# Kernel tuning notes

Hardware: AMD Instinct MI355X
Metric: run time of the kernel (lower is better)

The kernel has to match this reference:

```python
import jax, jax.numpy as jnp
import numpy as np

N = 100000
E = 1600000
H = 128
M = 256
L = 6
G = 512          # number of graphs in the batch
A = 95           # num_atom_types
EXTRA = 3        # input_dim - 1
EPS = 1e-5


def swish(x):
    return x * jax.nn.sigmoid(x)


def setup_inputs() -> dict:
    key = jax.random.key(0)
    ks = jax.random.split(key, 16)
    z = jax.random.randint(ks[0], (N, 1), 0, A).astype(jnp.float32)
    extra = jax.random.normal(ks[1], (N, EXTRA), dtype=jnp.float32)
    x = jnp.concatenate([z, extra], axis=1)                     # [N, 4]
    edge_index = jax.random.randint(ks[2], (2, E), 0, N)        # [2, E]
    batch = jnp.sort(jax.random.randint(ks[3], (N,), 0, G))     # [N]
    s = 0.02
    z_embed = jax.random.normal(ks[4], (A, H), dtype=jnp.float32) * s
    extra_w = jax.random.normal(ks[5], (H, EXTRA), dtype=jnp.float32) * (1.0 / np.sqrt(EXTRA))
    extra_b = jnp.zeros((H,), jnp.float32)
    conv_w = jax.random.normal(ks[6], (L, H, H), dtype=jnp.float32) * (1.0 / np.sqrt(H))
    conv_b = jnp.zeros((L, H), jnp.float32)
    gamma = jnp.ones((L, H), jnp.float32)
    beta = jnp.zeros((L, H), jnp.float32)
    mean_scale = jnp.ones((L, H), jnp.float32)
    mlp_w1 = jax.random.normal(ks[7], (L, M, H), dtype=jnp.float32) * (1.0 / np.sqrt(H))
    mlp_b1 = jnp.zeros((L, M), jnp.float32)
    mlp_w2 = jax.random.normal(ks[8], (L, H, M), dtype=jnp.float32) * (1.0 / np.sqrt(M))
    mlp_b2 = jnp.zeros((L, H), jnp.float32)
    return dict(x=x, edge_index=edge_index, batch=batch, z_embed=z_embed,
                extra_w=extra_w, extra_b=extra_b, conv_w=conv_w, conv_b=conv_b,
                gamma=gamma, beta=beta, mean_scale=mean_scale,
                mlp_w1=mlp_w1, mlp_b1=mlp_b1, mlp_w2=mlp_w2, mlp_b2=mlp_b2)


def gnn_forward(x, edge_index, batch, z_embed, extra_w, extra_b, conv_w, conv_b,
                gamma, beta, mean_scale, mlp_w1, mlp_b1, mlp_w2, mlp_b2):
    z = x[:, 0].astype(jnp.int32)
    h = z_embed[z] + x[:, 1:] @ extra_w.T + extra_b                 # [N, H]

    # GCN: add self loops, symmetric normalization (computed once; graph is static)
    loop = jnp.arange(N)
    src = jnp.concatenate([edge_index[0], loop])
    dst = jnp.concatenate([edge_index[1], loop])
    deg = jax.ops.segment_sum(jnp.ones_like(dst, jnp.float32), dst, num_segments=N)
    dinv = jnp.where(deg > 0, jax.lax.rsqrt(jnp.maximum(deg, 1.0)), 0.0)
    norm = (dinv[src] * dinv[dst])[:, None]                         # [E+N, 1]

    cnt = jax.ops.segment_sum(jnp.ones((N,), jnp.float32), batch, num_segments=G)[:, None]
    cnt = jnp.maximum(cnt, 1.0)

    for i in range(L):
        h_res = h
        # GCNConv
        xw = h @ conv_w[i].T
        agg = jax.ops.segment_sum(xw[src] * norm, dst, num_segments=N) + conv_b[i]
        # GraphNorm: gamma * (x - alpha*mean) / sqrt(var + eps) + beta, per graph
        mean = jax.ops.segment_sum(agg, batch, num_segments=G) / cnt   # [G, H]
        sub = agg - mean_scale[i] * mean[batch]
        var = jax.ops.segment_sum(sub * sub, batch, num_segments=G) / cnt
        hn = gamma[i] * sub * jax.lax.rsqrt(var[batch] + EPS) + beta[i]
        ha = swish(hn)
        # residual MLP
        h = swish(swish(ha @ mlp_w1[i].T + mlp_b1[i]) @ mlp_w2[i].T + mlp_b2[i]) + h_res
    return h


def reference(x, edge_index, batch, z_embed, extra_w, extra_b, conv_w, conv_b,
              gamma, beta, mean_scale, mlp_w1, mlp_b1, mlp_w2, mlp_b2):
    return gnn_forward(x, edge_index, batch, z_embed, extra_w, extra_b, conv_w, conv_b,
                       gamma, beta, mean_scale, mlp_w1, mlp_b1, mlp_w2, mlp_b2)
```

## Files before the change

kernel.cpp:

```cpp
#include <hip/hip_runtime.h>

#define NN 100000
#define EE 1600000
#define HH 128
#define MM 256
#define LL 6
#define GG 512
#define SCAN_NB ((NN + 1023) / 1024)

typedef __attribute__((ext_vector_type(8))) short short8;
typedef __attribute__((ext_vector_type(4))) float floatx4;

__device__ __forceinline__ float swishf(float v) {
    return v * __builtin_amdgcn_rcpf(1.0f + __expf(-v));
}

__device__ __forceinline__ unsigned short f2bf(float f) {
    unsigned u = __builtin_bit_cast(unsigned, f);
    unsigned r = u + 0x7FFFu + ((u >> 16) & 1u);
    return (unsigned short)(r >> 16);
}

__device__ __forceinline__ float bf2f(unsigned short u) {
    return __builtin_bit_cast(float, (unsigned)u << 16);
}

__device__ __forceinline__ float2 bf2f2(unsigned u) {
    float2 r;
    r.x = __builtin_bit_cast(float, u << 16);
    r.y = __builtin_bit_cast(float, u & 0xFFFF0000u);
    return r;
}

__device__ __forceinline__ unsigned cvt2bf(float a, float b) {
    unsigned r;
    asm("v_cvt_pk_bf16_f32 %0, %1, %2" : "=v"(r) : "v"(a), "v"(b));
    return r;
}

__device__ __forceinline__ void unpack8(uint4 v, float* a) {
    float2 p0 = bf2f2(v.x), p1 = bf2f2(v.y), p2 = bf2f2(v.z), p3 = bf2f2(v.w);
    a[0] = p0.x; a[1] = p0.y; a[2] = p1.x; a[3] = p1.y;
    a[4] = p2.x; a[5] = p2.y; a[6] = p3.x; a[7] = p3.y;
}

__device__ __forceinline__ uint4 pack8(const float* o) {
    uint4 pk;
    pk.x = cvt2bf(o[0], o[1]);
    pk.y = cvt2bf(o[2], o[3]);
    pk.z = cvt2bf(o[4], o[5]);
    pk.w = cvt2bf(o[6], o[7]);
    return pk;
}

__device__ __forceinline__ uint2 pack4(const float* o) {
    uint2 pk;
    pk.x = cvt2bf(o[0], o[1]);
    pk.y = cvt2bf(o[2], o[3]);
    return pk;
}

__global__ void k_embed(const float* __restrict__ x, const float* __restrict__ z_embed,
                        const float* __restrict__ ew, const float* __restrict__ eb,
                        unsigned short* __restrict__ hb) {
    int idx = blockIdx.x * blockDim.x + threadIdx.x;
    if (idx >= NN * 32) return;
    int n = idx >> 5;
    int c0 = (idx & 31) << 2;
    const float* xr = x + (size_t)n * 4;
    int z = (int)xr[0];
    float x1 = xr[1], x2 = xr[2], x3 = xr[3];
    const float* ze = z_embed + (size_t)z * HH + c0;
    float o[4];
#pragma unroll
    for (int j = 0; j < 4; ++j) {
        int c = c0 + j;
        o[j] = ze[j] + x1 * ew[c * 3 + 0] + x2 * ew[c * 3 + 1] + x3 * ew[c * 3 + 2] + eb[c];
    }
    *(uint2*)(hb + (size_t)n * HH + c0) = pack4(o);
}

__global__ void k_f2bf3(const float* __restrict__ s1, unsigned short* __restrict__ d1, int n1,
                        const float* __restrict__ s2, unsigned short* __restrict__ d2, int n2,
                        const float* __restrict__ s3, unsigned short* __restrict__ d3, int n3) {
    int i = blockIdx.x * blockDim.x + threadIdx.x;
    if (i < n1) {
        d1[i] = f2bf(s1[i]);
    } else if (i < n1 + n2) {
        d2[i - n1] = f2bf(s2[i - n1]);
    } else if (i < n1 + n2 + n3) {
        d3[i - n1 - n2] = f2bf(s3[i - n1 - n2]);
    }
}

__global__ __launch_bounds__(256) void k_degree_p(const int* __restrict__ dst,
                                                  int* __restrict__ deg) {
    int part = blockIdx.x & 7;
    int blk = blockIdx.x >> 3;
    int nb = gridDim.x >> 3;
    int lo = (int)((long long)part * NN / 8);
    int hi = (int)((long long)(part + 1) * NN / 8);
    for (int e = blk * 256 + threadIdx.x; e < EE; e += nb * 256) {
        int d = dst[e];
        if (d >= lo && d < hi) atomicAdd(&deg[d], 1);
    }
}

__global__ void k_scan1(const int* __restrict__ deg, int* __restrict__ bsum,
                        float* __restrict__ dinv) {
    __shared__ int sd[256];
    int t = threadIdx.x;
    int base = blockIdx.x * 1024 + t * 4;
    int s = 0;
#pragma unroll
    for (int j = 0; j < 4; ++j) {
        int i = base + j;
        if (i < NN) {
            int dg = deg[i];
            s += dg;
            dinv[i] = rsqrtf((float)(dg + 1));
        }
    }
    sd[t] = s;
    __syncthreads();
    for (int off = 128; off > 0; off >>= 1) {
        if (t < off) sd[t] += sd[t + off];
        __syncthreads();
    }
    if (t == 0) bsum[blockIdx.x] = sd[0];
}

__global__ void k_scan2(const int* __restrict__ bsum, int* __restrict__ boff) {
    __shared__ int sd[128];
    int t = threadIdx.x;
    int v = (t < SCAN_NB) ? bsum[t] : 0;
    sd[t] = v;
    __syncthreads();
    for (int off = 1; off < 128; off <<= 1) {
        int u = (t >= off) ? sd[t - off] : 0;
        __syncthreads();
        sd[t] += u;
        __syncthreads();
    }
    boff[t] = sd[t] - v;
}

__global__ void k_scan3(const int* __restrict__ deg, const int* __restrict__ boff,
                        int* __restrict__ rowptr) {
    __shared__ int sd[256];
    int t = threadIdx.x;
    int base = blockIdx.x * 1024 + t * 4;
    int v[4];
    int s = 0;
#pragma unroll
    for (int j = 0; j < 4; ++j) {
        int i = base + j;
        v[j] = (i < NN) ? deg[i] : 0;
        s += v[j];
    }
    sd[t] = s;
    __syncthreads();
    for (int off = 1; off < 256; off <<= 1) {
        int u = (t >= off) ? sd[t - off] : 0;
        __syncthreads();
        sd[t] += u;
        __syncthreads();
    }
    int run = boff[blockIdx.x] + sd[t] - s;
#pragma unroll
    for (int j = 0; j < 4; ++j) {
        int i = base + j;
        if (i < NN) rowptr[i] = run;
        if (i == NN - 1) rowptr[NN] = run + v[j];
        run += v[j];
    }
}

__global__ __launch_bounds__(256) void k_fill_p(const int* __restrict__ ei,
                                                const int* __restrict__ rowptr,
                                                int* __restrict__ cursor,
                                                int* __restrict__ col) {
    int part = blockIdx.x & 7;
    int blk = blockIdx.x >> 3;
    int nb = gridDim.x >> 3;
    int lo = (int)((long long)part * NN / 8);
    int hi = (int)((long long)(part + 1) * NN / 8);
    for (int e = blk * 256 + threadIdx.x; e < EE; e += nb * 256) {
        int d = ei[EE + e];
        if (d >= lo && d < hi) {
            int p = atomicAdd(&cursor[d], 1);
            col[rowptr[d] + p] = ei[e];
        }
    }
}

__global__ void k_gptr(const int* __restrict__ batch, int* __restrict__ gptr) {
    int n = blockIdx.x * blockDim.x + threadIdx.x;
    if (n >= NN) return;
    int b = batch[n];
    int pb = (n == 0) ? -1 : batch[n - 1];
    for (int g = pb + 1; g <= b; ++g) gptr[g] = n;
    if (n == NN - 1) {
        for (int g = b + 1; g <= GG; ++g) gptr[g] = NN;
    }
}

__global__ __launch_bounds__(256) void k_conv(const unsigned short* __restrict__ A,
                                              const unsigned short* __restrict__ B,
                                              const float* __restrict__ dinv,
                                              unsigned short* __restrict__ Cb) {
    __shared__ unsigned short Bs[128][HH + 8];
    const int tid = threadIdx.x;
    const int wave = tid >> 6;
    const int lane = tid & 63;
    const int quad = lane >> 4;
    const int l16 = lane & 15;
    const int wr = (wave & 1) << 6;
    const int wc = (wave >> 1) << 6;
    const int rowBase = blockIdx.x * 128;

    for (int i = tid; i < 128 * (HH / 8); i += 256) {
        int r = i / (HH / 8);
        int kk = (i % (HH / 8)) * 8;
        int rho = (r & 64) | ((r & 3) << 4) | ((r >> 2) & 15);
        *(uint4*)(&Bs[rho][kk]) = *(const uint4*)(B + (size_t)r * HH + kk);
    }

    floatx4 acc[4][4];
    const floatx4 zed = {0.f, 0.f, 0.f, 0.f};
#pragma unroll
    for (int i = 0; i < 4; ++i)
#pragma unroll
        for (int j = 0; j < 4; ++j) acc[i][j] = zed;

    int ar[4];
#pragma unroll
    for (int i = 0; i < 4; ++i) {
        int r = rowBase + wr + (i << 4) + l16;
        ar[i] = r < NN ? r : NN - 1;
    }

    __syncthreads();

#pragma unroll
    for (int ks = 0; ks < HH / 32; ++ks) {
        int k = (ks << 5) + (quad << 3);
        short8 a[4], b[4];
#pragma unroll
        for (int i = 0; i < 4; ++i) a[i] = *(const short8*)(A + (size_t)ar[i] * HH + k);
#pragma unroll
        for (int j = 0; j < 4; ++j) b[j] = *(const short8*)(&Bs[wc + (j << 4) + l16][k]);
#pragma unroll
        for (int i = 0; i < 4; ++i)
#pragma unroll
            for (int j = 0; j < 4; ++j)
                acc[i][j] =
                    __builtin_amdgcn_mfma_f32_16x16x32_bf16(a[i], b[j], acc[i][j], 0, 0, 0);
    }

    const int c0 = wc + (l16 << 2);
#pragma unroll
    for (int i = 0; i < 4; ++i) {
        int rb = rowBase + wr + (i << 4) + (quad << 2);
#pragma unroll
        for (int reg = 0; reg < 4; ++reg) {
            int r = rb + reg;
            if (r < NN) {
                float dv = dinv[r];
                float o[4];
#pragma unroll
                for (int j = 0; j < 4; ++j) o[j] = acc[i][j][reg] * dv;
                *(uint2*)(Cb + (size_t)r * HH + c0) = pack4(o);
            }
        }
    }
}

__global__ __launch_bounds__(256) void k_agg(const unsigned short* __restrict__ y,
                                             const int* __restrict__ rowptr,
                                             const int* __restrict__ col,
                                             const float* __restrict__ dinv,
                                             const float* __restrict__ cb,
                                             const int* __restrict__ batch,
                                             unsigned short* __restrict__ agg,
                                             float* __restrict__ S1g,
                                             float* __restrict__ S2g) {
    __shared__ float s1s[4][128];
    __shared__ float s2s[4][128];
    __shared__ int sg[4];
    int w = threadIdx.x >> 6;
    int lane = threadIdx.x & 63;
    int grp = lane >> 4;
    int l16 = lane & 15;
    const uint4* yv = (const uint4*)y;
    const int dbase = blockIdx.x * 16 + w * 4;

    float cbv[8];
    {
        float4 c0 = *(const float4*)(cb + l16 * 8);
        float4 c1 = *(const float4*)(cb + l16 * 8 + 4);
        cbv[0] = c0.x; cbv[1] = c0.y; cbv[2] = c0.z; cbv[3] = c0.w;
        cbv[4] = c1.x; cbv[5] = c1.y; cbv[6] = c1.z; cbv[7] = c1.w;
    }

    float sA[8], sB[8];
#pragma unroll
    for (int j = 0; j < 8; ++j) { sA[j] = 0.f; sB[j] = 0.f; }
    int gcur = -1;

    for (int i = 0; i < 4; ++i) {
        int d = dbase + i;
        float acc[8];
#pragma unroll
        for (int j = 0; j < 8; ++j) acc[j] = 0.f;
        if (grp == 0) {
            uint4 v = yv[(size_t)d * 16 + l16];
            unpack8(v, acc);
        }
        int beg = rowptr[d];
        int end = rowptr[d + 1];
        int e = beg + grp;
        for (; e + 4 < end; e += 8) {
            int s0 = col[e];
            int s1 = col[e + 4];
            uint4 v0 = yv[(size_t)s0 * 16 + l16];
            uint4 v1 = yv[(size_t)s1 * 16 + l16];
            float b0[8], b1[8];
            unpack8(v0, b0);
            unpack8(v1, b1);
#pragma unroll
            for (int k = 0; k < 8; ++k) acc[k] += (b0[k] + b1[k]);
        }
        if (e < end) {
            int s0 = col[e];
            uint4 v0 = yv[(size_t)s0 * 16 + l16];
            float b0[8];
            unpack8(v0, b0);
#pragma unroll
            for (int k = 0; k < 8; ++k) acc[k] += b0[k];
        }
#pragma unroll
        for (int j = 0; j < 8; ++j) {
            acc[j] += __shfl_xor(acc[j], 16, 64);
            acc[j] += __shfl_xor(acc[j], 32, 64);
        }
        if (grp == 0) {
            float dv = dinv[d];
            float o[8];
#pragma unroll
            for (int j = 0; j < 8; ++j) o[j] = acc[j] * dv + cbv[j];
            uint4 pk = pack8(o);
            *(uint4*)(agg + (size_t)d * HH + l16 * 8) = pk;
            float2 q0 = bf2f2(pk.x), q1 = bf2f2(pk.y), q2 = bf2f2(pk.z), q3 = bf2f2(pk.w);
            float orv[8] = {q0.x, q0.y, q1.x, q1.y, q2.x, q2.y, q3.x, q3.y};
            int g = batch[d];
            if (g != gcur) {
                if (gcur >= 0) {
#pragma unroll
                    for (int j = 0; j < 8; ++j) {
                        atomicAdd(&S1g[gcur * HH + l16 * 8 + j], sA[j]);
                        atomicAdd(&S2g[gcur * HH + l16 * 8 + j], sB[j]);
                    }
                }
                gcur = g;
#pragma unroll
                for (int j = 0; j < 8; ++j) {
                    sA[j] = orv[j];
                    sB[j] = orv[j] * orv[j];
                }
            } else {
#pragma unroll
                for (int j = 0; j < 8; ++j) {
                    sA[j] += orv[j];
                    sB[j] += orv[j] * orv[j];
                }
            }
        }
    }

    if (grp == 0) {
#pragma unroll
        for (int j = 0; j < 8; ++j) {
            s1s[w][l16 * 8 + j] = sA[j];
            s2s[w][l16 * 8 + j] = sB[j];
        }
        if (l16 == 0) sg[w] = gcur;
    }
    __syncthreads();
    if (threadIdx.x < 128) {
        int c = threadIdx.x;
        int g0 = sg[0], g1 = sg[1], g2 = sg[2], g3 = sg[3];
        if (g0 >= 0 && g0 == g1 && g0 == g2 && g0 == g3) {
            float a = (s1s[0][c] + s1s[1][c]) + (s1s[2][c] + s1s[3][c]);
            float b = (s2s[0][c] + s2s[1][c]) + (s2s[2][c] + s2s[3][c]);
            atomicAdd(&S1g[g0 * HH + c], a);
            atomicAdd(&S2g[g0 * HH + c], b);
        } else {
            int gs[4] = {g0, g1, g2, g3};
#pragma unroll
            for (int ww = 0; ww < 4; ++ww) {
                if (gs[ww] >= 0) {
                    atomicAdd(&S1g[gs[ww] * HH + c], s1s[ww][c]);
                    atomicAdd(&S2g[gs[ww] * HH + c], s2s[ww][c]);
                }
            }
        }
    }
}

__global__ __launch_bounds__(128) void k_finalize(const int* __restrict__ gptr,
                                                  const float* __restrict__ ms,
                                                  const float* __restrict__ gamma,
                                                  const float* __restrict__ beta,
                                                  const float* __restrict__ S1g,
                                                  const float* __restrict__ S2g,
                                                  float* __restrict__ c1,
                                                  float* __restrict__ c0) {
    int g = blockIdx.x;
    int c = threadIdx.x;
    int cnt = gptr[g + 1] - gptr[g];
    float inv = 1.0f / (float)(cnt > 0 ? cnt : 1);
    float S1 = S1g[g * HH + c];
    float S2 = S2g[g * HH + c];
    float m = S1 * inv;
    float msc = ms[c];
    float var = S2 * inv - msc * (2.0f - msc) * m * m;
    float rstd = rsqrtf(var + 1e-5f);
    float c1v = gamma[c] * rstd;
    c1[g * HH + c] = c1v;
    c0[g * HH + c] = beta[c] - c1v * msc * m;
}

__global__ __launch_bounds__(256, 4) void k_mega(const unsigned short* __restrict__ agg,
                                                 const int* __restrict__ batch,
                                                 const float* __restrict__ c1,
                                                 const float* __restrict__ c0,
                                                 const unsigned short* __restrict__ W1,
                                                 const float* __restrict__ b1,
                                                 const unsigned short* __restrict__ W2,
                                                 const float* __restrict__ b2,
                                                 const unsigned short* __restrict__ Wc,
                                                 const float* __restrict__ dinv,
                                                 unsigned short* __restrict__ hb,
                                                 float* __restrict__ h_out,
                                                 unsigned short* __restrict__ y_out,
                                                 int writeF, int doConv) {
    __shared__ unsigned short ha_s[64 * 136];
    __shared__ unsigned short ts[64 * 136];
    const int tid = threadIdx.x;
    const int wave = tid >> 6;
    const int lane = tid & 63;
    const int quad = lane >> 4;
    const int l16 = lane & 15;
    const int rowBase = blockIdx.x * 64;
    const floatx4 zed = {0.f, 0.f, 0.f, 0.f};

    const int wrb = (wave & 1) << 5;
    const int wcb = (wave >> 1) << 6;
    const int co = wcb + (l16 << 2);

    {
        int lr = tid >> 2;
        int coff = (tid & 3) << 5;
        int r = rowBase + lr;
        if (r >= NN) r = NN - 1;
        int g = batch[r];
        const float* c1p = c1 + g * HH + coff;
        const float* c0p = c0 + g * HH + coff;
#pragma unroll
        for (int q = 0; q < 4; ++q) {
            uint4 raw = *(const uint4*)(agg + (size_t)r * HH + coff + (q << 3));
            float v[8];
            unpack8(raw, v);
            float4 ca = *(const float4*)(c1p + (q << 3));
            float4 cb4 = *(const float4*)(c1p + (q << 3) + 4);
            float4 da = *(const float4*)(c0p + (q << 3));
            float4 db = *(const float4*)(c0p + (q << 3) + 4);
            float cc1[8] = {ca.x, ca.y, ca.z, ca.w, cb4.x, cb4.y, cb4.z, cb4.w};
            float cc0[8] = {da.x, da.y, da.z, da.w, db.x, db.y, db.z, db.w};
            float o[8];
#pragma unroll
            for (int j = 0; j < 8; ++j) o[j] = swishf(cc1[j] * v[j] + cc0[j]);
            *(uint4*)(&ha_s[lr * 136 + coff + (q << 3)]) = pack8(o);
        }
    }
    __syncthreads();

    {
        floatx4 acc2[2][4];
#pragma unroll
        for (int i = 0; i < 2; ++i)
#pragma unroll
            for (int j = 0; j < 4; ++j) acc2[i][j] = zed;

#pragma unroll
        for (int h = 0; h < 2; ++h) {
            floatx4 acc1[4][2];
#pragma unroll
            for (int i = 0; i < 4; ++i)
#pragma unroll
                for (int j = 0; j < 2; ++j) acc1[i][j] = zed;
            const int tcol = (wave << 5) + (l16 << 1);
#pragma unroll
            for (int ks = 0; ks < 4; ++ks) {
                int k = (ks << 5) + (quad << 3);
                short8 a[4], b[2];
#pragma unroll
                for (int i = 0; i < 4; ++i)
                    a[i] = *(const short8*)(&ha_s[((i << 4) + l16) * 136 + k]);
#pragma unroll
                for (int j = 0; j < 2; ++j)
                    b[j] = *(const short8*)(W1 + (size_t)((h << 7) + tcol + j) * HH + k);
#pragma unroll
                for (int i = 0; i < 4; ++i)
#pragma unroll
                    for (int j = 0; j < 2; ++j)
                        acc1[i][j] = __builtin_amdgcn_mfma_f32_16x16x32_bf16(a[i], b[j],
                                                                             acc1[i][j], 0, 0, 0);
            }
            float2 bv = *(const float2*)(b1 + (h << 7) + tcol);
#pragma unroll
            for (int i = 0; i < 4; ++i) {
#pragma unroll
                for (int reg = 0; reg < 4; ++reg) {
                    int lr = (i << 4) + (quad << 2) + reg;
                    float o0 = swishf(acc1[i][0][reg] + bv.x);
                    float o1 = swishf(acc1[i][1][reg] + bv.y);
                    *(unsigned*)(&ts[lr * 136 + tcol]) = cvt2bf(o0, o1);
                }
            }
            __syncthreads();

#pragma unroll
            for (int ks = 0; ks < 4; ++ks) {
                int k = (ks << 5) + (quad << 3);
                short8 a[2], b[4];
#pragma unroll
                for (int i = 0; i < 2; ++i)
                    a[i] = *(const short8*)(&ts[(wrb + (i << 4) + l16) * 136 + k]);
#pragma unroll
                for (int j = 0; j < 4; ++j)
                    b[j] = *(const short8*)(W2 + (size_t)(wcb + (l16 << 2) + j) * MM +
                                            (h << 7) + k);
#pragma unroll
                for (int i = 0; i < 2; ++i)
#pragma unroll
                    for (int j = 0; j < 4; ++j)
                        acc2[i][j] = __builtin_amdgcn_mfma_f32_16x16x32_bf16(a[i], b[j],
                                                                             acc2[i][j], 0, 0, 0);
            }
            if (h == 0) __syncthreads();
        }

        float4 b4 = *(const float4*)(b2 + co);
        float bv[4] = {b4.x, b4.y, b4.z, b4.w};
#pragma unroll
        for (int i = 0; i < 2; ++i) {
#pragma unroll
            for (int reg = 0; reg < 4; ++reg) {
                int lr = wrb + (i << 4) + (quad << 2) + reg;
                int r = rowBase + lr;
                if (r < NN) {
                    uint2 rv = *(const uint2*)(hb + (size_t)r * HH + co);
                    float2 r01 = bf2f2(rv.x), r23 = bf2f2(rv.y);
                    float o[4];
                    o[0] = swishf(acc2[i][0][reg] + bv[0]) + r01.x;
                    o[1] = swishf(acc2[i][1][reg] + bv[1]) + r01.y;
                    o[2] = swishf(acc2[i][2][reg] + bv[2]) + r23.x;
                    o[3] = swishf(acc2[i][3][reg] + bv[3]) + r23.y;
                    if (doConv) {
                        uint2 pk = pack4(o);
                        *(uint2*)(hb + (size_t)r * HH + co) = pk;
                        *(uint2*)(&ha_s[lr * 136 + co]) = pk;
                    } else {
                        *(float4*)(h_out + (size_t)r * HH + co) =
                            make_float4(o[0], o[1], o[2], o[3]);
                    }
                } else if (doConv) {
                    *(uint2*)(&ha_s[lr * 136 + co]) = make_uint2(0u, 0u);
                }
            }
        }
    }

    if (doConv) {
        __syncthreads();
        floatx4 acc3[2][4];
#pragma unroll
        for (int i = 0; i < 2; ++i)
#pragma unroll
            for (int j = 0; j < 4; ++j) acc3[i][j] = zed;
#pragma unroll
        for (int ks = 0; ks < 4; ++ks) {
            int k = (ks << 5) + (quad << 3);
            short8 a[2], b[4];
#pragma unroll
            for (int i = 0; i < 2; ++i)
                a[i] = *(const short8*)(&ha_s[(wrb + (i << 4) + l16) * 136 + k]);
#pragma unroll
            for (int j = 0; j < 4; ++j)
                b[j] = *(const short8*)(Wc + (size_t)(wcb + (l16 << 2) + j) * HH + k);
#pragma unroll
            for (int i = 0; i < 2; ++i)
#pragma unroll
                for (int j = 0; j < 4; ++j)
                    acc3[i][j] =
                        __builtin_amdgcn_mfma_f32_16x16x32_bf16(a[i], b[j], acc3[i][j], 0, 0, 0);
        }
#pragma unroll
        for (int i = 0; i < 2; ++i) {
#pragma unroll
            for (int reg = 0; reg < 4; ++reg) {
                int r = rowBase + wrb + (i << 4) + (quad << 2) + reg;
                if (r < NN) {
                    float dv = dinv[r];
                    float o[4];
#pragma unroll
                    for (int j = 0; j < 4; ++j) o[j] = acc3[i][j][reg] * dv;
                    *(uint2*)(y_out + (size_t)r * HH + co) = pack4(o);
                }
            }
        }
    }
}

extern "C" void kernel_launch(void* const* d_in, const int* in_sizes, int n_in,
                              void* d_out, int out_size, void* d_ws, size_t ws_size,
                              hipStream_t stream) {
    const float* x = (const float*)d_in[0];
    const int* ei = (const int*)d_in[1];
    const int* batch = (const int*)d_in[2];
    const float* z_embed = (const float*)d_in[3];
    const float* extra_w = (const float*)d_in[4];
    const float* extra_b = (const float*)d_in[5];
    const float* conv_w = (const float*)d_in[6];
    const float* conv_b = (const float*)d_in[7];
    const float* gamma = (const float*)d_in[8];
    const float* beta = (const float*)d_in[9];
    const float* mean_scale = (const float*)d_in[10];
    const float* mlp_w1 = (const float*)d_in[11];
    const float* mlp_b1 = (const float*)d_in[12];
    const float* mlp_w2 = (const float*)d_in[13];
    const float* mlp_b2 = (const float*)d_in[14];
    float* h_out = (float*)d_out;

    char* wsB = (char*)d_ws;
    size_t off = 0;
    auto alloc = [&](size_t bytes) -> void* {
        void* p = (void*)(wsB + off);
        off = (off + bytes + 255) & ~(size_t)255;
        return p;
    };
    float* dinv = (float*)alloc((size_t)NN * 4);
    int* deg = (int*)alloc((size_t)NN * 4);
    int* cursor = (int*)alloc((size_t)NN * 4);
    int* rowptr = (int*)alloc((size_t)(NN + 1) * 4);
    int* bsum = (int*)alloc(128 * 4);
    int* boff = (int*)alloc(128 * 4);
    int* col = (int*)alloc((size_t)EE * 4);
    int* gptr = (int*)alloc((size_t)(GG + 1) * 4);
    float* c1t = (float*)alloc((size_t)GG * HH * 4);
    float* c0t = (float*)alloc((size_t)GG * HH * 4);
    float* S1g6 = (float*)alloc((size_t)LL * GG * HH * 4);
    float* S2g6 = (float*)alloc((size_t)LL * GG * HH * 4);
    unsigned short* wb =
        (unsigned short*)alloc((size_t)(LL * (HH * HH + MM * HH + HH * MM)) * 2);
    unsigned short* cwb = wb;
    unsigned short* w1b = wb + (size_t)LL * HH * HH;
    unsigned short* w2b = w1b + (size_t)LL * MM * HH;
    unsigned short* hb = (unsigned short*)alloc((size_t)NN * HH * 2);
    unsigned short* ybuf = (unsigned short*)alloc((size_t)NN * HH * 2);
    unsigned short* aggb = (unsigned short*)alloc((size_t)NN * HH * 2);

    hipMemsetAsync(deg, 0, (size_t)NN * 4, stream);
    hipMemsetAsync(cursor, 0, (size_t)NN * 4, stream);
    hipMemsetAsync(S1g6, 0, (size_t)LL * GG * HH * 4, stream);
    hipMemsetAsync(S2g6, 0, (size_t)LL * GG * HH * 4, stream);

    k_embed<<<(NN * 32 + 255) / 256, 256, 0, stream>>>(x, z_embed, extra_w, extra_b, hb);
    {
        int n1 = LL * HH * HH, n2 = LL * MM * HH, n3 = LL * HH * MM;
        int nt = n1 + n2 + n3;
        k_f2bf3<<<(nt + 255) / 256, 256, 0, stream>>>(conv_w, cwb, n1, mlp_w1, w1b, n2,
                                                      mlp_w2, w2b, n3);
    }
    k_degree_p<<<1024, 256, 0, stream>>>(ei + EE, deg);
    k_scan1<<<SCAN_NB, 256, 0, stream>>>(deg, bsum, dinv);
    k_scan2<<<1, 128, 0, stream>>>(bsum, boff);
    k_scan3<<<SCAN_NB, 256, 0, stream>>>(deg, boff, rowptr);
    k_fill_p<<<1024, 256, 0, stream>>>(ei, rowptr, cursor, col);
    k_gptr<<<(NN + 255) / 256, 256, 0, stream>>>(batch, gptr);

    int gconv = (NN + 127) / 128;
    int gmega = (NN + 63) / 64;
    k_conv<<<gconv, 256, 0, stream>>>(hb, cwb, dinv, ybuf);
    for (int i = 0; i < LL; ++i) {
        float* S1 = S1g6 + (size_t)i * GG * HH;
        float* S2 = S2g6 + (size_t)i * GG * HH;
        k_agg<<<NN / 16, 256, 0, stream>>>(ybuf, rowptr, col, dinv,
                                           conv_b + (size_t)i * HH, batch, aggb, S1, S2);
        k_finalize<<<GG, 128, 0, stream>>>(gptr, mean_scale + (size_t)i * HH,
                                           gamma + (size_t)i * HH, beta + (size_t)i * HH,
                                           S1, S2, c1t, c0t);
        k_mega<<<gmega, 256, 0, stream>>>(
            aggb, batch, c1t, c0t, w1b + (size_t)i * MM * HH, mlp_b1 + (size_t)i * MM,
            w2b + (size_t)i * HH * MM, mlp_b2 + (size_t)i * HH,
            cwb + (size_t)(i + 1 < LL ? i + 1 : 0) * HH * HH, dinv, hb, h_out, ybuf,
            i == LL - 1 ? 1 : 0, i < LL - 1 ? 1 : 0);
    }
}
```

Baseline: 1.222 ms.

## Reorder GCN as aggregate-then-transform, fusing conv matmul into aggregation kernel

```diff
diff --git a/kernel.cpp b/kernel.cpp
--- a/kernel.cpp
+++ b/kernel.cpp
@@ -205,95 +205,29 @@
     }
 }
 
-__global__ __launch_bounds__(256) void k_conv(const unsigned short* __restrict__ A,
-                                              const unsigned short* __restrict__ B,
-                                              const float* __restrict__ dinv,
-                                              unsigned short* __restrict__ Cb) {
-    __shared__ unsigned short Bs[128][HH + 8];
-    const int tid = threadIdx.x;
-    const int wave = tid >> 6;
-    const int lane = tid & 63;
-    const int quad = lane >> 4;
-    const int l16 = lane & 15;
-    const int wr = (wave & 1) << 6;
-    const int wc = (wave >> 1) << 6;
-    const int rowBase = blockIdx.x * 128;
-
-    for (int i = tid; i < 128 * (HH / 8); i += 256) {
-        int r = i / (HH / 8);
-        int kk = (i % (HH / 8)) * 8;
-        int rho = (r & 64) | ((r & 3) << 4) | ((r >> 2) & 15);
-        *(uint4*)(&Bs[rho][kk]) = *(const uint4*)(B + (size_t)r * HH + kk);
-    }
-
-    floatx4 acc[4][4];
-    const floatx4 zed = {0.f, 0.f, 0.f, 0.f};
-#pragma unroll
-    for (int i = 0; i < 4; ++i)
-#pragma unroll
-        for (int j = 0; j < 4; ++j) acc[i][j] = zed;
-
-    int ar[4];
-#pragma unroll
-    for (int i = 0; i < 4; ++i) {
-        int r = rowBase + wr + (i << 4) + l16;
-        ar[i] = r < NN ? r : NN - 1;
-    }
-
-    __syncthreads();
-
-#pragma unroll
-    for (int ks = 0; ks < HH / 32; ++ks) {
-        int k = (ks << 5) + (quad << 3);
-        short8 a[4], b[4];
-#pragma unroll
-        for (int i = 0; i < 4; ++i) a[i] = *(const short8*)(A + (size_t)ar[i] * HH + k);
-#pragma unroll
-        for (int j = 0; j < 4; ++j) b[j] = *(const short8*)(&Bs[wc + (j << 4) + l16][k]);
-#pragma unroll
-        for (int i = 0; i < 4; ++i)
-#pragma unroll
-            for (int j = 0; j < 4; ++j)
-                acc[i][j] =
-                    __builtin_amdgcn_mfma_f32_16x16x32_bf16(a[i], b[j], acc[i][j], 0, 0, 0);
-    }
-
-    const int c0 = wc + (l16 << 2);
-#pragma unroll
-    for (int i = 0; i < 4; ++i) {
-        int rb = rowBase + wr + (i << 4) + (quad << 2);
-#pragma unroll
-        for (int reg = 0; reg < 4; ++reg) {
-            int r = rb + reg;
-            if (r < NN) {
-                float dv = dinv[r];
-                float o[4];
-#pragma unroll
-                for (int j = 0; j < 4; ++j) o[j] = acc[i][j][reg] * dv;
-                *(uint2*)(Cb + (size_t)r * HH + c0) = pack4(o);
-            }
-        }
-    }
-}
-
-__global__ __launch_bounds__(256) void k_agg(const unsigned short* __restrict__ y,
+__global__ __launch_bounds__(256) void k_agg(const unsigned short* __restrict__ h,
                                              const int* __restrict__ rowptr,
                                              const int* __restrict__ col,
                                              const float* __restrict__ dinv,
+                                             const unsigned short* __restrict__ Wc,
                                              const float* __restrict__ cb,
                                              const int* __restrict__ batch,
                                              unsigned short* __restrict__ agg,
                                              float* __restrict__ S1g,
                                              float* __restrict__ S2g) {
+    __shared__ unsigned short gs[16 * 136];
+    __shared__ float s_agg[16 * 132];
     __shared__ float s1s[4][128];
     __shared__ float s2s[4][128];
     __shared__ int sg[4];
-    int w = threadIdx.x >> 6;
-    int lane = threadIdx.x & 63;
-    int grp = lane >> 4;
-    int l16 = lane & 15;
-    const uint4* yv = (const uint4*)y;
+    const int tid = threadIdx.x;
+    const int w = tid >> 6;
+    const int lane = tid & 63;
+    const int grp = lane >> 4;
+    const int l16 = lane & 15;
+    const uint4* yv = (const uint4*)h;
     const int dbase = blockIdx.x * 16 + w * 4;
+    const floatx4 zed = {0.f, 0.f, 0.f, 0.f};
 
     float cbv[8];
     {
@@ -303,11 +237,6 @@
         cbv[4] = c1.x; cbv[5] = c1.y; cbv[6] = c1.z; cbv[7] = c1.w;
     }
 
-    float sA[8], sB[8];
-#pragma unroll
-    for (int j = 0; j < 8; ++j) { sA[j] = 0.f; sB[j] = 0.f; }
-    int gcur = -1;
-
     for (int i = 0; i < 4; ++i) {
         int d = dbase + i;
         float acc[8];
@@ -315,29 +244,36 @@
         for (int j = 0; j < 8; ++j) acc[j] = 0.f;
         if (grp == 0) {
             uint4 v = yv[(size_t)d * 16 + l16];
-            unpack8(v, acc);
+            float b0[8];
+            unpack8(v, b0);
+            float dv = dinv[d];
+#pragma unroll
+            for (int k2 = 0; k2 < 8; ++k2) acc[k2] = dv * b0[k2];
         }
         int beg = rowptr[d];
         int end = rowptr[d + 1];
         int e = beg + grp;
         for (; e + 4 < end; e += 8) {
             int s0 = col[e];
-            int s1 = col[e + 4];
+            int s1i = col[e + 4];
+            float dv0 = dinv[s0];
+            float dv1 = dinv[s1i];
             uint4 v0 = yv[(size_t)s0 * 16 + l16];
-            uint4 v1 = yv[(size_t)s1 * 16 + l16];
+            uint4 v1 = yv[(size_t)s1i * 16 + l16];
             float b0[8], b1[8];
             unpack8(v0, b0);
             unpack8(v1, b1);
 #pragma unroll
-            for (int k = 0; k < 8; ++k) acc[k] += (b0[k] + b1[k]);
+            for (int k2 = 0; k2 < 8; ++k2) acc[k2] += dv0 * b0[k2] + dv1 * b1[k2];
         }
         if (e < end) {
             int s0 = col[e];
+            float dv0 = dinv[s0];
             uint4 v0 = yv[(size_t)s0 * 16 + l16];
             float b0[8];
             unpack8(v0, b0);
 #pragma unroll
-            for (int k = 0; k < 8; ++k) acc[k] += b0[k];
+            for (int k2 = 0; k2 < 8; ++k2) acc[k2] += dv0 * b0[k2];
         }
 #pragma unroll
         for (int j = 0; j < 8; ++j) {
@@ -345,10 +281,45 @@
             acc[j] += __shfl_xor(acc[j], 32, 64);
         }
         if (grp == 0) {
+            *(uint4*)(&gs[(w * 4 + i) * 136 + l16 * 8]) = pack8(acc);
+        }
+    }
+    __syncthreads();
+
+    {
+        const int bcol = (w << 5) + (l16 << 1);
+        floatx4 acc1[2];
+        acc1[0] = zed;
+        acc1[1] = zed;
+#pragma unroll
+        for (int ks = 0; ks < 4; ++ks) {
+            int k = (ks << 5) + (grp << 3);
+            short8 a = *(const short8*)(&gs[l16 * 136 + k]);
+            short8 bf0 = *(const short8*)(Wc + (size_t)bcol * HH + k);
+            short8 bf1 = *(const short8*)(Wc + (size_t)(bcol + 1) * HH + k);
+            acc1[0] = __builtin_amdgcn_mfma_f32_16x16x32_bf16(a, bf0, acc1[0], 0, 0, 0);
+            acc1[1] = __builtin_amdgcn_mfma_f32_16x16x32_bf16(a, bf1, acc1[1], 0, 0, 0);
+        }
+#pragma unroll
+        for (int j = 0; j < 2; ++j)
+#pragma unroll
+            for (int reg = 0; reg < 4; ++reg)
+                s_agg[(grp * 4 + reg) * 132 + bcol + j] = acc1[j][reg];
+    }
+    __syncthreads();
+
+    float sA[8], sB[8];
+#pragma unroll
+    for (int j = 0; j < 8; ++j) { sA[j] = 0.f; sB[j] = 0.f; }
+    int gcur = -1;
+    for (int i = 0; i < 4; ++i) {
+        int d = dbase + i;
+        if (grp == 0) {
             float dv = dinv[d];
             float o[8];
 #pragma unroll
-            for (int j = 0; j < 8; ++j) o[j] = acc[j] * dv + cbv[j];
+            for (int j = 0; j < 8; ++j)
+                o[j] = s_agg[(w * 4 + i) * 132 + l16 * 8 + j] * dv + cbv[j];
             uint4 pk = pack8(o);
             *(uint4*)(agg + (size_t)d * HH + l16 * 8) = pk;
             float2 q0 = bf2f2(pk.x), q1 = bf2f2(pk.y), q2 = bf2f2(pk.z), q3 = bf2f2(pk.w);
@@ -377,7 +348,6 @@
             }
         }
     }
-
     if (grp == 0) {
 #pragma unroll
         for (int j = 0; j < 8; ++j) {
@@ -396,12 +366,12 @@
             atomicAdd(&S1g[g0 * HH + c], a);
             atomicAdd(&S2g[g0 * HH + c], b);
         } else {
-            int gs[4] = {g0, g1, g2, g3};
+            int gsx[4] = {g0, g1, g2, g3};
 #pragma unroll
             for (int ww = 0; ww < 4; ++ww) {
-                if (gs[ww] >= 0) {
-                    atomicAdd(&S1g[gs[ww] * HH + c], s1s[ww][c]);
-                    atomicAdd(&S2g[gs[ww] * HH + c], s2s[ww][c]);
+                if (gsx[ww] >= 0) {
+                    atomicAdd(&S1g[gsx[ww] * HH + c], s1s[ww][c]);
+                    atomicAdd(&S2g[gsx[ww] * HH + c], s2s[ww][c]);
                 }
             }
         }
@@ -439,12 +409,9 @@
                                                  const float* __restrict__ b1,
                                                  const unsigned short* __restrict__ W2,
                                                  const float* __restrict__ b2,
-                                                 const unsigned short* __restrict__ Wc,
-                                                 const float* __restrict__ dinv,
                                                  unsigned short* __restrict__ hb,
                                                  float* __restrict__ h_out,
-                                                 unsigned short* __restrict__ y_out,
-                                                 int writeF, int doConv) {
+                                                 int last) {
     __shared__ unsigned short ha_s[64 * 136];
     __shared__ unsigned short ts[64 * 136];
     const int tid = threadIdx.x;
@@ -568,56 +535,12 @@
                     o[1] = swishf(acc2[i][1][reg] + bv[1]) + r01.y;
                     o[2] = swishf(acc2[i][2][reg] + bv[2]) + r23.x;
                     o[3] = swishf(acc2[i][3][reg] + bv[3]) + r23.y;
-                    if (doConv) {
-                        uint2 pk = pack4(o);
-                        *(uint2*)(hb + (size_t)r * HH + co) = pk;
-                        *(uint2*)(&ha_s[lr * 136 + co]) = pk;
+                    if (!last) {
+                        *(uint2*)(hb + (size_t)r * HH + co) = pack4(o);
                     } else {
                         *(float4*)(h_out + (size_t)r * HH + co) =
                             make_float4(o[0], o[1], o[2], o[3]);
                     }
-                } else if (doConv) {
-                    *(uint2*)(&ha_s[lr * 136 + co]) = make_uint2(0u, 0u);
-                }
-            }
-        }
-    }
-
-    if (doConv) {
-        __syncthreads();
-        floatx4 acc3[2][4];
-#pragma unroll
-        for (int i = 0; i < 2; ++i)
-#pragma unroll
-            for (int j = 0; j < 4; ++j) acc3[i][j] = zed;
-#pragma unroll
-        for (int ks = 0; ks < 4; ++ks) {
-            int k = (ks << 5) + (quad << 3);
-            short8 a[2], b[4];
-#pragma unroll
-            for (int i = 0; i < 2; ++i)
-                a[i] = *(const short8*)(&ha_s[(wrb + (i << 4) + l16) * 136 + k]);
-#pragma unroll
-            for (int j = 0; j < 4; ++j)
-                b[j] = *(const short8*)(Wc + (size_t)(wcb + (l16 << 2) + j) * HH + k);
-#pragma unroll
-            for (int i = 0; i < 2; ++i)
-#pragma unroll
-                for (int j = 0; j < 4; ++j)
-                    acc3[i][j] =
-                        __builtin_amdgcn_mfma_f32_16x16x32_bf16(a[i], b[j], acc3[i][j], 0, 0, 0);
-        }
-#pragma unroll
-        for (int i = 0; i < 2; ++i) {
-#pragma unroll
-            for (int reg = 0; reg < 4; ++reg) {
-                int r = rowBase + wrb + (i << 4) + (quad << 2) + reg;
-                if (r < NN) {
-                    float dv = dinv[r];
-                    float o[4];
-#pragma unroll
-                    for (int j = 0; j < 4; ++j) o[j] = acc3[i][j][reg] * dv;
-                    *(uint2*)(y_out + (size_t)r * HH + co) = pack4(o);
                 }
             }
         }
@@ -669,7 +592,6 @@
     unsigned short* w1b = wb + (size_t)LL * HH * HH;
     unsigned short* w2b = w1b + (size_t)LL * MM * HH;
     unsigned short* hb = (unsigned short*)alloc((size_t)NN * HH * 2);
-    unsigned short* ybuf = (unsigned short*)alloc((size_t)NN * HH * 2);
     unsigned short* aggb = (unsigned short*)alloc((size_t)NN * HH * 2);
 
     hipMemsetAsync(deg, 0, (size_t)NN * 4, stream);
@@ -691,21 +613,19 @@
     k_fill_p<<<1024, 256, 0, stream>>>(ei, rowptr, cursor, col);
     k_gptr<<<(NN + 255) / 256, 256, 0, stream>>>(batch, gptr);
 
-    int gconv = (NN + 127) / 128;
     int gmega = (NN + 63) / 64;
-    k_conv<<<gconv, 256, 0, stream>>>(hb, cwb, dinv, ybuf);
     for (int i = 0; i < LL; ++i) {
         float* S1 = S1g6 + (size_t)i * GG * HH;
         float* S2 = S2g6 + (size_t)i * GG * HH;
-        k_agg<<<NN / 16, 256, 0, stream>>>(ybuf, rowptr, col, dinv,
+        k_agg<<<NN / 16, 256, 0, stream>>>(hb, rowptr, col, dinv,
+                                           cwb + (size_t)i * HH * HH,
                                            conv_b + (size_t)i * HH, batch, aggb, S1, S2);
         k_finalize<<<GG, 128, 0, stream>>>(gptr, mean_scale + (size_t)i * HH,
                                            gamma + (size_t)i * HH, beta + (size_t)i * HH,
                                            S1, S2, c1t, c0t);
         k_mega<<<gmega, 256, 0, stream>>>(
             aggb, batch, c1t, c0t, w1b + (size_t)i * MM * HH, mlp_b1 + (size_t)i * MM,
-            w2b + (size_t)i * HH * MM, mlp_b2 + (size_t)i * HH,
-            cwb + (size_t)(i + 1 < LL ? i + 1 : 0) * HH * HH, dinv, hb, h_out, ybuf,
-            i == LL - 1 ? 1 : 0, i < LL - 1 ? 1 : 0);
-    }
-}
+            w2b + (size_t)i * HH * MM, mlp_b2 + (size_t)i * HH, hb, h_out,
+            i == LL - 1 ? 1 : 0);
+    }
+}
```

Result: slower. 1.260 ms (+3.1%).
